# Kernel tuning notes

Hardware: AMD Instinct MI355X
Metric: run time of the kernel (lower is better)

The kernel has to match this reference:

```python
import jax, jax.numpy as jnp
import numpy as np

DIM = 1024      # internal_dim
HEADS = 16
HD = DIM // HEADS
M = 256         # meaning_dim (protected prefix)
E = 4           # num_experts
K = 2           # top_k
HID = 2048      # dim * ffn_mult
MID = 2048      # DeepNarrow mid = 2*dim
LB = 0.01
EPS = 1.1920929e-07  # torch.finfo(float32).eps (nn.RMSNorm default)


def _rms(x, w):
    return x * jax.lax.rsqrt(jnp.mean(x * x, axis=-1, keepdims=True) + EPS) * w


def _gelu(x):
    return jax.nn.gelu(x, approximate=False)  # F.gelu default (erf)


def setup_inputs() -> dict:
    key = jax.random.key(0)
    ks = jax.random.split(key, 20)
    d = DIM
    w = lambda k, s: (jax.random.normal(k, s, jnp.float32) * 0.02)
    return {
        "x": jax.random.normal(ks[0], (4, 1024, d), jnp.float32),
        "n1_w": jnp.ones((d,), jnp.float32),
        "n2_w": jnp.ones((d,), jnp.float32),
        "wq": w(ks[1], (d, d)), "wk": w(ks[2], (d, d)),
        "wv": w(ks[3], (d, d)), "wo": w(ks[4], (d, d)),
        "qn_w": jnp.ones((HD,), jnp.float32), "kn_w": jnp.ones((HD,), jnp.float32),
        "gate_w": w(ks[5], (E, d)),
        # expert 0: StandardFFN
        "e0_up": w(ks[6], (HID, d)), "e0_down": w(ks[7], (d, HID)),
        # expert 1: SwiGLUFFN
        "e1_w1": w(ks[8], (HID, d)), "e1_w2": w(ks[9], (HID, d)), "e1_down": w(ks[10], (d, HID)),
        # expert 2: DeepNarrowFFN
        "e2_l1": w(ks[11], (MID, d)), "e2_l2": w(ks[12], (HID, MID)),
        "e2_l3": w(ks[13], (MID, HID)), "e2_l4": w(ks[14], (d, MID)),
        # expert 3: BottleneckFFN (neck = dim)
        "e3_down": w(ks[15], (d, d)), "e3_up": w(ks[16], (HID, d)), "e3_out": w(ks[17], (d, HID)),
    }


def reference(x, n1_w, n2_w, wq, wk, wv, wo, qn_w, kn_w, gate_w,
              e0_up, e0_down, e1_w1, e1_w2, e1_down,
              e2_l1, e2_l2, e2_l3, e2_l4, e3_down, e3_up, e3_out):
    B, T, C = x.shape
    # ---- attention with QK-norm, causal (NoPE) ----
    h = _rms(x, n1_w)
    heads = lambda w_: (h @ w_.T).reshape(B, T, HEADS, HD).transpose(0, 2, 1, 3)  # [B,H,T,hd]
    q = _rms(heads(wq), qn_w)
    k = _rms(heads(wk), kn_w)
    v = heads(wv)
    scores = jnp.einsum('bhqd,bhkd->bhqk', q, k) * (HD ** -0.5)
    causal = jnp.tril(jnp.ones((T, T), bool))
    scores = jnp.where(causal[None, None], scores, -jnp.inf)
    attn = jax.nn.softmax(scores, axis=-1)
    ao = jnp.einsum('bhqk,bhkd->bhqd', attn, v).transpose(0, 2, 1, 3).reshape(B, T, C) @ wo.T
    ao = ao.at[:, :, :M].set(0.0)  # protect meaning dims
    x = x + ao
    # ---- heterogeneous MoE, top-k routing ----
    xf = _rms(x, n2_w).reshape(-1, C)  # [N,C]
    N = xf.shape[0]
    logits = jnp.nan_to_num(xf @ gate_w.T)
    probs = jax.nn.softmax(logits, axis=-1)
    topv, topi = jax.lax.top_k(probs, K)
    topv = topv / (topv.sum(-1, keepdims=True) + 1e-8)
    # dense per-token combine weights: zero for unselected experts (same math as dispatch loop)
    wts = jnp.zeros((N, E), x.dtype).at[jnp.arange(N)[:, None], topi].add(topv)
    o0 = _gelu(xf @ e0_up.T) @ e0_down.T
    o1 = (jax.nn.silu(xf @ e1_w1.T) * (xf @ e1_w2.T)) @ e1_down.T
    o2 = _gelu(_gelu(_gelu(xf @ e2_l1.T) @ e2_l2.T) @ e2_l3.T) @ e2_l4.T
    o3 = _gelu(_gelu(xf @ e3_down.T) @ e3_up.T) @ e3_out.T
    moe = (wts[:, 0:1] * o0 + wts[:, 1:2] * o1 + wts[:, 2:3] * o2 + wts[:, 3:4] * o3)
    moe = moe.reshape(B, T, C).at[:, :, :M].set(0.0)
    return x + moe
```

## Files before the change

kernel.cpp:

```cpp
#include <hip/hip_runtime.h>
#include <math.h>

#define DIM   1024
#define NTOK  4096
#define TSEQ  1024
#define NHEAD 16
#define MPROT 256
#define EPSR  1.1920929e-07f
#define SA    64.0f
#define SW    256.0f
#define SPC   64.0f

typedef __attribute__((ext_vector_type(8))) short          short8;
typedef __attribute__((ext_vector_type(8))) _Float16       half8;
typedef __attribute__((ext_vector_type(4))) _Float16       half4;
typedef __attribute__((ext_vector_type(4))) float          f32x4;
typedef __attribute__((ext_vector_type(4))) unsigned short us4;

static __device__ __forceinline__ float bf2f(unsigned short s) {
  union { unsigned int u; float f; } c; c.u = ((unsigned int)s) << 16; return c.f;
}
static __device__ __forceinline__ unsigned short f2bf(float f) {
  union { float f; unsigned int u; } c; c.f = f;
  return (unsigned short)((c.u + 0x7fffu + ((c.u >> 16) & 1u)) >> 16);
}
static __device__ __forceinline__ void gload16(void* lds, const void* g) {
  __builtin_amdgcn_global_load_lds(
      (__attribute__((address_space(1))) void*)const_cast<void*>(g),
      (__attribute__((address_space(3))) void*)lds, 16, 0, 0);
}

static __device__ __forceinline__ void tile_swz(int& m0, int& n0) {
  const int gx = gridDim.x;
  const int L = blockIdx.y * gx + blockIdx.x;
  const int xcd = L & 7;
  const int j = L >> 3;
  const int mbq = j / gx;
  const int nb = j - mbq * gx;
  m0 = ((mbq << 3) | xcd) << 7;
  n0 = nb << 7;
}

__global__ __launch_bounds__(256) void cvt_attn4_k(const float* __restrict__ wq,
                                                   const float* __restrict__ wk,
                                                   const float* __restrict__ wv,
                                                   const float* __restrict__ wo,
                                                   _Float16* __restrict__ dh,
                                                   _Float16* __restrict__ dl) {
  const int wi = blockIdx.y;
  const float* s = (wi == 0) ? wq : (wi == 1) ? wk : (wi == 2) ? wv : wo;
  const int i = blockIdx.x * 256 + threadIdx.x;
  const size_t off4 = ((size_t)wi << 20) >> 2;
  const float4 v = ((const float4*)s)[i];
  float a0 = v.x * SW, a1 = v.y * SW, a2 = v.z * SW, a3 = v.w * SW;
  half4 hv, lv;
  _Float16 h0 = (_Float16)a0; hv[0] = h0; lv[0] = (_Float16)(a0 - (float)h0);
  _Float16 h1 = (_Float16)a1; hv[1] = h1; lv[1] = (_Float16)(a1 - (float)h1);
  _Float16 h2 = (_Float16)a2; hv[2] = h2; lv[2] = (_Float16)(a2 - (float)h2);
  _Float16 h3 = (_Float16)a3; hv[3] = h3; lv[3] = (_Float16)(a3 - (float)h3);
  ((half4*)dh)[off4 + i] = hv; ((half4*)dl)[off4 + i] = lv;
}

__global__ __launch_bounds__(256) void cvt_moe_all_k(
    const float* s0, const float* s1, const float* s2, const float* s3,
    const float* s4, const float* s5, const float* s6, const float* s7,
    const float* s8, const float* s9, const float* s10, const float* s11,
    unsigned short* __restrict__ dst) {
  const int n4tab[12] = {524288, 524288, 524288, 524288, 524288, 524288,
                         1048576, 1048576, 524288, 262144, 524288, 524288};
  const size_t offtab[12] = {0, 2097152, 4194304, 6291456, 8388608, 10485760,
                             12582912, 16777216, 20971520, 23068672, 24117248, 26214400};
  const int wi = blockIdx.y;
  const int i = blockIdx.x * 256 + threadIdx.x;
  if (i >= n4tab[wi]) return;
  const float* s;
  switch (wi) {
    case 0: s = s0; break; case 1: s = s1; break; case 2: s = s2; break;
    case 3: s = s3; break; case 4: s = s4; break; case 5: s = s5; break;
    case 6: s = s6; break; case 7: s = s7; break; case 8: s = s8; break;
    case 9: s = s9; break; case 10: s = s10; break; default: s = s11; break;
  }
  const float4 v = ((const float4*)s)[i];
  us4 o; o[0] = f2bf(v.x); o[1] = f2bf(v.y); o[2] = f2bf(v.z); o[3] = f2bf(v.w);
  ((us4*)(dst + offtab[wi]))[i] = o;
}

__global__ __launch_bounds__(256) void rms_split_k(const float* __restrict__ in,
                                                   const float* __restrict__ wgt,
                                                   _Float16* __restrict__ oh,
                                                   _Float16* __restrict__ ol) {
  const int row = blockIdx.x, tid = threadIdx.x;
  const float4 v = ((const float4*)(in + (size_t)row * DIM))[tid];
  float ss = v.x * v.x + v.y * v.y + v.z * v.z + v.w * v.w;
#pragma unroll
  for (int o = 32; o; o >>= 1) ss += __shfl_xor(ss, o);
  __shared__ float red[4];
  if ((tid & 63) == 0) red[tid >> 6] = ss;
  __syncthreads();
  const float sc = rsqrtf((red[0] + red[1] + red[2] + red[3]) * (1.0f / DIM) + EPSR) * SA;
  const float4 wv = ((const float4*)wgt)[tid];
  float a[4] = {v.x * sc * wv.x, v.y * sc * wv.y, v.z * sc * wv.z, v.w * sc * wv.w};
  half4 hv, lv;
#pragma unroll
  for (int j = 0; j < 4; ++j) {
    _Float16 hh = (_Float16)a[j]; hv[j] = hh; lv[j] = (_Float16)(a[j] - (float)hh);
  }
  ((half4*)(oh + (size_t)row * DIM))[tid] = hv;
  ((half4*)(ol + (size_t)row * DIM))[tid] = lv;
}

__global__ __launch_bounds__(256) void rmsgate_k(const float* __restrict__ x2,
                                                 const float* __restrict__ n2w,
                                                 const float* __restrict__ gw,
                                                 unsigned short* __restrict__ xfb,
                                                 float* __restrict__ wts,
                                                 float* __restrict__ moe) {
  const int row = blockIdx.x, tid = threadIdx.x;
  ((float4*)(moe + (size_t)row * DIM))[tid] = (float4){0.f, 0.f, 0.f, 0.f};
  const float4 v = ((const float4*)(x2 + (size_t)row * DIM))[tid];
  float ss = v.x * v.x + v.y * v.y + v.z * v.z + v.w * v.w;
#pragma unroll
  for (int o = 32; o; o >>= 1) ss += __shfl_xor(ss, o);
  __shared__ float red[4];
  __shared__ float redE[4][4];
  const int w = tid >> 6, lane = tid & 63;
  if (lane == 0) red[w] = ss;
  __syncthreads();
  const float sc = rsqrtf((red[0] + red[1] + red[2] + red[3]) * (1.0f / DIM) + EPSR);
  const float4 nw = ((const float4*)n2w)[tid];
  const float xn0 = v.x * sc * nw.x, xn1 = v.y * sc * nw.y;
  const float xn2 = v.z * sc * nw.z, xn3 = v.w * sc * nw.w;
  us4 ob; ob[0] = f2bf(xn0); ob[1] = f2bf(xn1); ob[2] = f2bf(xn2); ob[3] = f2bf(xn3);
  ((us4*)(xfb + (size_t)row * DIM))[tid] = ob;
#pragma unroll
  for (int e = 0; e < 4; ++e) {
    const float4 g = ((const float4*)(gw + (size_t)e * DIM))[tid];
    float d = xn0 * g.x + xn1 * g.y + xn2 * g.z + xn3 * g.w;
#pragma unroll
    for (int o = 32; o; o >>= 1) d += __shfl_xor(d, o);
    if (lane == 0) redE[w][e] = d;
  }
  __syncthreads();
  if (tid == 0) {
    float lg[4];
#pragma unroll
    for (int e = 0; e < 4; ++e) lg[e] = redE[0][e] + redE[1][e] + redE[2][e] + redE[3][e];
    const float mx = fmaxf(fmaxf(lg[0], lg[1]), fmaxf(lg[2], lg[3]));
    float pe[4]; float sum = 0.0f;
#pragma unroll
    for (int e = 0; e < 4; ++e) { pe[e] = __expf(lg[e] - mx); sum += pe[e]; }
#pragma unroll
    for (int e = 0; e < 4; ++e) pe[e] /= sum;
    int i1 = 0;
    for (int e = 1; e < 4; ++e) if (pe[e] > pe[i1]) i1 = e;
    int i2 = -1;
    for (int e = 0; e < 4; ++e) { if (e == i1) continue; if (i2 < 0 || pe[e] > pe[i2]) i2 = e; }
    const float s2 = pe[i1] + pe[i2] + 1e-8f;
    float o[4] = {0.f, 0.f, 0.f, 0.f};
    o[i1] = pe[i1] / s2; o[i2] = pe[i2] / s2;
    float4 r; r.x = o[0]; r.y = o[1]; r.z = o[2]; r.w = o[3];
    *(float4*)(wts + (size_t)row * 4) = r;
  }
}

__global__ __launch_bounds__(256) void qknorm2_k(_Float16* __restrict__ qh,
                                                 _Float16* __restrict__ ql,
                                                 _Float16* __restrict__ kh,
                                                 _Float16* __restrict__ kl,
                                                 const float* __restrict__ qnw,
                                                 const float* __restrict__ knw) {
  _Float16* ph; _Float16* pl; const float* wgt;
  if (blockIdx.y == 0) { ph = qh; pl = ql; wgt = qnw; }
  else { ph = kh; pl = kl; wgt = knw; }
  const int idx = (blockIdx.x << 2) + (threadIdx.x >> 6);
  const int lane = threadIdx.x & 63;
  const size_t off = ((size_t)idx << 6) + lane;
  const float v = (float)ph[off] + (float)pl[off];
  float ss = v * v;
#pragma unroll
  for (int o = 32; o; o >>= 1) ss += __shfl_xor(ss, o);
  const float sc = rsqrtf(ss * (1.0f / (64.0f * SA * SA)) + EPSR);
  const float nv = v * sc * wgt[lane];
  _Float16 hh = (_Float16)nv;
  ph[off] = hh; pl[off] = (_Float16)(nv - (float)hh);
}

__global__ __launch_bounds__(256) void route2_k(const float* __restrict__ wts,
                                                int* __restrict__ idxP,
                                                int* __restrict__ meta) {
  const int tid = threadIdx.x, w = tid >> 6, lane = tid & 63;
  __shared__ int wsum[4];
  __shared__ int baseS;
  int off = 0;
  for (int e = 0; e < 4; ++e) {
    if (tid == 0) baseS = 0;
    __syncthreads();
    for (int c = 0; c < 16; ++c) {
      const int tok = (c << 8) + tid;
      const bool pred = wts[(size_t)tok * 4 + e] > 0.0f;
      const unsigned long long m = __ballot(pred);
      const int lanepre = __popcll(m & ((1ull << lane) - 1ull));
      if (lane == 0) wsum[w] = __popcll(m);
      __syncthreads();
      int wpre = 0;
#pragma unroll
      for (int i = 0; i < 4; ++i) wpre += (i < w) ? wsum[i] : 0;
      const int tot = wsum[0] + wsum[1] + wsum[2] + wsum[3];
      if (pred) idxP[off + baseS + wpre + lanepre] = tok;
      __syncthreads();
      if (tid == 0) baseS += tot;
      __syncthreads();
    }
    const int cnt = baseS;
    const int padded = (cnt + 127) & ~127;
    for (int j = cnt + tid; j < padded; j += 256) idxP[off + j] = -1;
    if (tid == 0) meta[80 + e] = off;
    const int mb0 = off >> 7, nmb = padded >> 7;
    for (int j = tid; j < nmb; j += 256) meta[mb0 + j] = e;
    off += padded;
    __syncthreads();
  }
  for (int j = (off >> 7) + tid; j < 72; j += 256) meta[j] = -1;
}

struct SubOpP {
  const unsigned short* A;
  const unsigned short* Bw;
  unsigned short* outb;
  const unsigned short* other;
  int K, nbn, act, ep, gath;
};
struct PhaseP { SubOpP op[4]; };

__global__ __launch_bounds__(256, 4) void gemm_moe_k(PhaseP ph,
                                                     const int* __restrict__ meta,
                                                     const int* __restrict__ idxP,
                                                     const float* __restrict__ wts,
                                                     float* __restrict__ moe) {
  __shared__ unsigned short As[128][64];
  __shared__ unsigned short Bs[128][64];
  const int L = blockIdx.y * 16 + blockIdx.x;
  const int xcd = L & 7;
  const int j = L >> 3;
  const int nb = j & 15;
  const int mb = ((j >> 4) << 3) | xcd;
  const int e = meta[mb];
  if (e < 0) return;
  SubOpP op;
  switch (e) {
    case 0: op = ph.op[0]; break;
    case 1: op = ph.op[1]; break;
    case 2: op = ph.op[2]; break;
    default: op = ph.op[3]; break;
  }
  if (op.nbn == 0 || nb >= op.nbn) return;
  const int m0p = mb << 7;
  const int lr0 = m0p - meta[80 + e];
  const int n0 = nb << 7;
  const int F = op.nbn << 7;
  const int K = op.K;
  const int tid = threadIdx.x;
  const int w = tid >> 6, lane = tid & 63;
  const int wr = ((w >> 1) << 6), wc = ((w & 1) << 6);
  const int rr = lane & 15, kgl = lane >> 4;
  const int srow = tid >> 3, sslot = tid & 7;

  int grow[4];
#pragma unroll
  for (int i = 0; i < 4; ++i) {
    const int r = (i << 5) + srow;
    if (op.gath) {
      const int t = idxP[m0p + r];
      grow[i] = (t < 0) ? 0 : t;
    } else {
      grow[i] = lr0 + r;
    }
  }

  f32x4 acc[4][4];
#pragma unroll
  for (int a_ = 0; a_ < 4; ++a_)
#pragma unroll
    for (int b_ = 0; b_ < 4; ++b_) acc[a_][b_] = (f32x4){0.f, 0.f, 0.f, 0.f};

  const int KT = K >> 6;
  for (int kt = 0; kt < KT; ++kt) {
    const int k0 = kt << 6;
#pragma unroll
    for (int i = 0; i < 4; ++i) {
      const int r = (i << 5) + srow;
      const int ls = sslot ^ (r & 7);
      gload16(&As[(i << 5) + (w << 3)][0], op.A + (size_t)grow[i] * K + k0 + (ls << 3));
      gload16(&Bs[(i << 5) + (w << 3)][0], op.Bw + (size_t)(n0 + r) * K + k0 + (ls << 3));
    }
    __syncthreads();
    short8 af[4][2], bfr[4][2];
#pragma unroll
    for (int f = 0; f < 4; ++f) {
#pragma unroll
      for (int ks = 0; ks < 2; ++ks) {
        const int row = wr + (f << 4) + rr;
        const int kg = (ks << 2) + kgl;
        af[f][ks] = *(const short8*)&As[row][(kg ^ (row & 7)) << 3];
        const int col = wc + (f << 4) + rr;
        bfr[f][ks] = *(const short8*)&Bs[col][(kg ^ (col & 7)) << 3];
      }
    }
#pragma unroll
    for (int fi = 0; fi < 4; ++fi)
#pragma unroll
      for (int fj = 0; fj < 4; ++fj)
#pragma unroll
        for (int ks = 0; ks < 2; ++ks)
          acc[fi][fj] = __builtin_amdgcn_mfma_f32_16x16x32_bf16(
              af[fi][ks], bfr[fj][ks], acc[fi][fj], 0, 0, 0);
    __syncthreads();
  }
#pragma unroll
  for (int fi = 0; fi < 4; ++fi)
#pragma unroll
    for (int fj = 0; fj < 4; ++fj) {
      const int col = n0 + wc + (fj << 4) + rr;
#pragma unroll
      for (int r = 0; r < 4; ++r) {
        const int rl = wr + (fi << 4) + (kgl << 2) + r;
        float v = acc[fi][fj][r];
        if (op.act) v = 0.5f * v * (1.0f + erff(v * 0.70710678118654752f));
        if (op.ep == 0) {
          op.outb[(size_t)(lr0 + rl) * F + col] = f2bf(v);
        } else if (op.ep == 1) {
          const size_t off = (size_t)(lr0 + rl) * F + col;
          const float sv = v / (1.0f + __expf(-v));
          op.outb[off] = f2bf(sv * bf2f(op.other[off]));
        } else {
          const int tok = idxP[m0p + rl];
          if (tok >= 0)
            atomicAdd(&moe[(size_t)tok * DIM + col], wts[(size_t)tok * 4 + e] * v);
        }
      }
    }
}

template <int EP>
__global__ __launch_bounds__(256, 4) void gemm_split_k(
    const _Float16* __restrict__ Ah, const _Float16* __restrict__ Al,
    const _Float16* __restrict__ Bh, const _Float16* __restrict__ Bl,
    int K, int F,
    _Float16* __restrict__ Oh, _Float16* __restrict__ Ol, float oscale,
    const float* __restrict__ resid, float* __restrict__ outf,
    _Float16* __restrict__ K2h, _Float16* __restrict__ K2l,
    _Float16* __restrict__ V2h, _Float16* __restrict__ V2l) {
  __shared__ _Float16 AsH[128][32], AsL[128][32];
  __shared__ _Float16 BsH[128][32], BsL[128][32];
  const int tid = threadIdx.x;
  const int w = tid >> 6, lane = tid & 63;
  const int wr = ((w >> 1) << 6), wc = ((w & 1) << 6);
  int m0, n0;
  tile_swz(m0, n0);
  const int rr = lane & 15, kgl = lane >> 4;
  const int srow = tid >> 2, sslot = tid & 3;

  f32x4 acc[4][4];
#pragma unroll
  for (int a_ = 0; a_ < 4; ++a_)
#pragma unroll
    for (int b_ = 0; b_ < 4; ++b_) acc[a_][b_] = (f32x4){0.f, 0.f, 0.f, 0.f};

  const int KT = K >> 5;
  for (int kt = 0; kt < KT; ++kt) {
    const int k0 = kt << 5;
#pragma unroll
    for (int i = 0; i < 2; ++i) {
      const int r = (i << 6) + srow;
      const int ls = sslot ^ ((r >> 1) & 3);
      const size_t ga = (size_t)(m0 + r) * K + k0 + (ls << 3);
      const size_t gb = (size_t)(n0 + r) * K + k0 + (ls << 3);
      const int lr = (i << 6) + (w << 4);
      gload16(&AsH[lr][0], Ah + ga);
      gload16(&AsL[lr][0], Al + ga);
      gload16(&BsH[lr][0], Bh + gb);
      gload16(&BsL[lr][0], Bl + gb);
    }
    __syncthreads();
    half8 ah[4], al[4], bh[4], bl[4];
#pragma unroll
    for (int f = 0; f < 4; ++f) {
      const int row = wr + (f << 4) + rr;
      const int pa = (kgl ^ ((row >> 1) & 3)) << 3;
      ah[f] = *(const half8*)&AsH[row][pa];
      al[f] = *(const half8*)&AsL[row][pa];
      const int col = wc + (f << 4) + rr;
      const int pb = (kgl ^ ((col >> 1) & 3)) << 3;
      bh[f] = *(const half8*)&BsH[col][pb];
      bl[f] = *(const half8*)&BsL[col][pb];
    }
#pragma unroll
    for (int fi = 0; fi < 4; ++fi)
#pragma unroll
      for (int fj = 0; fj < 4; ++fj) {
        acc[fi][fj] = __builtin_amdgcn_mfma_f32_16x16x32_f16(ah[fi], bh[fj], acc[fi][fj], 0, 0, 0);
        acc[fi][fj] = __builtin_amdgcn_mfma_f32_16x16x32_f16(ah[fi], bl[fj], acc[fi][fj], 0, 0, 0);
        acc[fi][fj] = __builtin_amdgcn_mfma_f32_16x16x32_f16(al[fi], bh[fj], acc[fi][fj], 0, 0, 0);
      }
    __syncthreads();
  }
#pragma unroll
  for (int fi = 0; fi < 4; ++fi)
#pragma unroll
    for (int fj = 0; fj < 4; ++fj) {
      const int col = n0 + wc + (fj << 4) + rr;
      const int rowb = m0 + wr + (fi << 4) + (kgl << 2);
      if (EP == 3) {
        if (col < 2048) {
          _Float16* ph = (col < 1024) ? Oh : K2h;
          _Float16* pl = (col < 1024) ? Ol : K2l;
          const int c = col & 1023;
#pragma unroll
          for (int r = 0; r < 4; ++r) {
            const float v = acc[fi][fj][r] * oscale;
            const _Float16 hh2 = (_Float16)v;
            const size_t off = (size_t)(rowb + r) * DIM + c;
            ph[off] = hh2; pl[off] = (_Float16)(v - (float)hh2);
          }
        } else {
          const int c2 = col - 2048;
          half4 h4, l4;
#pragma unroll
          for (int r = 0; r < 4; ++r) {
            const float v = acc[fi][fj][r] * oscale;
            const _Float16 hh2 = (_Float16)v;
            h4[r] = hh2; l4[r] = (_Float16)(v - (float)hh2);
          }
          const size_t vt = ((size_t)((rowb >> 10) << 4) + (size_t)(c2 >> 6)) * 65536 +
                            (size_t)(c2 & 63) * 1024 + (size_t)(rowb & 1023);
          *(half4*)&V2h[vt] = h4;
          *(half4*)&V2l[vt] = l4;
        }
      } else {
#pragma unroll
        for (int r = 0; r < 4; ++r) {
          const size_t off = (size_t)(rowb + r) * F + col;
          const float v = acc[fi][fj][r] * oscale;
          outf[off] = resid[off] + (col >= MPROT ? v : 0.0f);
        }
      }
    }
}

__global__ __launch_bounds__(256, 2) void attn_k(
    const _Float16* __restrict__ Qh, const _Float16* __restrict__ Ql,
    const _Float16* __restrict__ Kh, const _Float16* __restrict__ Kl,
    const _Float16* __restrict__ Vth, const _Float16* __restrict__ Vtl,
    _Float16* __restrict__ Oh, _Float16* __restrict__ Ol) {
  __shared__ _Float16 Ksh[2][32][64], Ksl[2][32][64];
  __shared__ _Float16 Vsh[2][64][40], Vsl[2][64][40];
  __shared__ _Float16 Plh[4][16][40], Pll[4][16][40];
  const int n = blockIdx.x;
  const int qt = n >> 6;
  const int bh = ((n & 7) << 3) | ((n >> 3) & 7);
  const int b = bh >> 4, h = bh & 15;
  const int tid = threadIdx.x, w = tid >> 6, lane = tid & 63;
  const int rr = lane & 15, rg = lane >> 4;
  const size_t tokbase = (size_t)b * TSEQ;
  const int hcol = h << 6;
  const size_t vtbase = (size_t)bh << 16;
  const int q0w = (qt << 7) + (w << 5);
  const float sscale = 0.125f / (SA * SA);

  half8 qfh[2][2], qfl[2][2];
#pragma unroll
  for (int qf = 0; qf < 2; ++qf)
#pragma unroll
    for (int ks = 0; ks < 2; ++ks) {
      const size_t off = (tokbase + q0w + (qf << 4) + rr) * DIM + hcol + (ks << 5) + (rg << 3);
      qfh[qf][ks] = *(const half8*)&Qh[off];
      qfl[qf][ks] = *(const half8*)&Ql[off];
    }

  f32x4 oacc[2][4];
#pragma unroll
  for (int qf = 0; qf < 2; ++qf)
#pragma unroll
    for (int dg = 0; dg < 4; ++dg) oacc[qf][dg] = (f32x4){0.f, 0.f, 0.f, 0.f};
  float mreg[2] = {-INFINITY, -INFINITY}, lreg[2] = {0.f, 0.f};

  const int kr = (w << 3) + (lane >> 3);
  const int kswz = ((lane & 7) ^ (kr & 7)) << 3;
  const int vr = tid >> 2;
  const int vs = (tid & 3) << 3;

  const int ntiles = (qt + 1) << 2;

  {
    gload16(&Ksh[0][w << 3][0], &Kh[(tokbase + kr) * DIM + hcol + kswz]);
    gload16(&Ksl[0][w << 3][0], &Kl[(tokbase + kr) * DIM + hcol + kswz]);
    const half8 vvh = *(const half8*)&Vth[vtbase + (size_t)vr * TSEQ + vs];
    const half8 vvl = *(const half8*)&Vtl[vtbase + (size_t)vr * TSEQ + vs];
    *(half8*)&Vsh[0][vr][vs] = vvh;
    *(half8*)&Vsl[0][vr][vs] = vvl;
    __syncthreads();
  }

  for (int t = 0; t < ntiles; ++t) {
    const int cur = t & 1;
    const int kv0 = t << 5;
    const bool havenext = (t + 1 < ntiles);
    half8 nvh, nvl;
    if (havenext) {
      const int kn = kv0 + 32;
      gload16(&Ksh[cur ^ 1][w << 3][0], &Kh[(tokbase + kn + kr) * DIM + hcol + kswz]);
      gload16(&Ksl[cur ^ 1][w << 3][0], &Kl[(tokbase + kn + kr) * DIM + hcol + kswz]);
      nvh = *(const half8*)&Vth[vtbase + (size_t)vr * TSEQ + kn + vs];
      nvl = *(const half8*)&Vtl[vtbase + (size_t)vr * TSEQ + kn + vs];
    }
    if (kv0 <= q0w + 31) {
      half8 kfh[2][2], kfl[2][2];
#pragma unroll
      for (int kt = 0; kt < 2; ++kt)
#pragma unroll
        for (int ks = 0; ks < 2; ++ks) {
          const int row = (kt << 4) + rr;
          const int sw = ((((ks << 2) + rg)) ^ (row & 7)) << 3;
          kfh[kt][ks] = *(const half8*)&Ksh[cur][row][sw];
          kfl[kt][ks] = *(const half8*)&Ksl[cur][row][sw];
        }
#pragma unroll
      for (int qf = 0; qf < 2; ++qf) {
        if (kv0 > q0w + (qf << 4) + 15) continue;
        f32x4 st[2];
        st[0] = (f32x4){0.f, 0.f, 0.f, 0.f};
        st[1] = (f32x4){0.f, 0.f, 0.f, 0.f};
#pragma unroll
        for (int kt = 0; kt < 2; ++kt)
#pragma unroll
          for (int ks = 0; ks < 2; ++ks) {
            st[kt] = __builtin_amdgcn_mfma_f32_16x16x32_f16(kfh[kt][ks], qfh[qf][ks], st[kt], 0, 0, 0);
            st[kt] = __builtin_amdgcn_mfma_f32_16x16x32_f16(kfh[kt][ks], qfl[qf][ks], st[kt], 0, 0, 0);
            st[kt] = __builtin_amdgcn_mfma_f32_16x16x32_f16(kfl[kt][ks], qfh[qf][ks], st[kt], 0, 0, 0);
          }
        const int qg = q0w + (qf << 4) + rr;
        float s[2][4]; float mx = -INFINITY;
#pragma unroll
        for (int kt = 0; kt < 2; ++kt)
#pragma unroll
          for (int r = 0; r < 4; ++r) {
            float sv = st[kt][r] * sscale;
            if (kv0 + (kt << 4) + (rg << 2) + r > qg) sv = -INFINITY;
            s[kt][r] = sv; mx = fmaxf(mx, sv);
          }
        mx = fmaxf(mx, __shfl_xor(mx, 16));
        mx = fmaxf(mx, __shfl_xor(mx, 32));
        const float mn = fmaxf(mreg[qf], mx);
        const float al = __expf(mreg[qf] - mn);
        mreg[qf] = mn;
        float p[2][4]; float rs = 0.f;
#pragma unroll
        for (int kt = 0; kt < 2; ++kt)
#pragma unroll
          for (int r = 0; r < 4; ++r) { p[kt][r] = __expf(s[kt][r] - mn); rs += p[kt][r]; }
        rs += __shfl_xor(rs, 16);
        rs += __shfl_xor(rs, 32);
        lreg[qf] = lreg[qf] * al + rs;
#pragma unroll
        for (int kt = 0; kt < 2; ++kt) {
          half4 h4, l4;
#pragma unroll
          for (int r = 0; r < 4; ++r) {
            const float pv = p[kt][r] * SPC;
            const _Float16 ph = (_Float16)pv;
            h4[r] = ph; l4[r] = (_Float16)(pv - (float)ph);
          }
          *(half4*)&Plh[w][rr][(kt << 4) + (rg << 2)] = h4;
          *(half4*)&Pll[w][rr][(kt << 4) + (rg << 2)] = l4;
        }
        float alr[4];
#pragma unroll
        for (int r = 0; r < 4; ++r) alr[r] = __shfl(al, (lane & 48) | ((rg << 2) + r));
#pragma unroll
        for (int dg = 0; dg < 4; ++dg)
#pragma unroll
          for (int r = 0; r < 4; ++r) oacc[qf][dg][r] *= alr[r];
        const half8 pah = *(const half8*)&Plh[w][rr][rg << 3];
        const half8 pal = *(const half8*)&Pll[w][rr][rg << 3];
#pragma unroll
        for (int dg = 0; dg < 4; ++dg) {
          const half8 vfh2 = *(const half8*)&Vsh[cur][(dg << 4) + rr][rg << 3];
          const half8 vfl2 = *(const half8*)&Vsl[cur][(dg << 4) + rr][rg << 3];
          oacc[qf][dg] = __builtin_amdgcn_mfma_f32_16x16x32_f16(pah, vfh2, oacc[qf][dg], 0, 0, 0);
          oacc[qf][dg] = __builtin_amdgcn_mfma_f32_16x16x32_f16(pah, vfl2, oacc[qf][dg], 0, 0, 0);
          oacc[qf][dg] = __builtin_amdgcn_mfma_f32_16x16x32_f16(pal, vfh2, oacc[qf][dg], 0, 0, 0);
        }
      }
    }
    if (havenext) {
      *(half8*)&Vsh[cur ^ 1][vr][vs] = nvh;
      *(half8*)&Vsl[cur ^ 1][vr][vs] = nvl;
    }
    __syncthreads();
  }
#pragma unroll
  for (int qf = 0; qf < 2; ++qf) {
    float li[4];
#pragma unroll
    for (int r = 0; r < 4; ++r)
      li[r] = __shfl(lreg[qf], (lane & 48) | ((rg << 2) + r));
#pragma unroll
    for (int dg = 0; dg < 4; ++dg)
#pragma unroll
      for (int r = 0; r < 4; ++r) {
        const int qloc = (rg << 2) + r;
        const float ov = oacc[qf][dg][r] / (li[r] * SPC);
        const _Float16 hh2 = (_Float16)ov;
        const size_t off = (tokbase + q0w + (qf << 4) + qloc) * DIM + hcol + (dg << 4) + rr;
        Oh[off] = hh2;
        Ol[off] = (_Float16)(ov - (float)hh2);
      }
  }
}

__global__ __launch_bounds__(256) void comb_k(float* __restrict__ outp,
                                              const float* __restrict__ moe) {
  const size_t i = (size_t)blockIdx.x * 256 + threadIdx.x;
  const int c4 = (int)(i & 255);
  if (c4 >= 64) {
    float4 o = ((float4*)outp)[i];
    const float4 m = ((const float4*)moe)[i];
    o.x += m.x; o.y += m.y; o.z += m.z; o.w += m.w;
    ((float4*)outp)[i] = o;
  }
}

extern "C" void kernel_launch(void* const* d_in, const int* in_sizes, int n_in,
                              void* d_out, int out_size, void* d_ws, size_t ws_size,
                              hipStream_t stream) {
  (void)in_sizes; (void)n_in; (void)out_size; (void)ws_size;
  const float* x    = (const float*)d_in[0];
  const float* n1w  = (const float*)d_in[1];
  const float* n2w  = (const float*)d_in[2];
  const float* wq   = (const float*)d_in[3];
  const float* wk   = (const float*)d_in[4];
  const float* wv   = (const float*)d_in[5];
  const float* wo   = (const float*)d_in[6];
  const float* qnw  = (const float*)d_in[7];
  const float* knw  = (const float*)d_in[8];
  const float* gw   = (const float*)d_in[9];
  const float* moesrc[12] = {
    (const float*)d_in[10], (const float*)d_in[11],
    (const float*)d_in[12], (const float*)d_in[13], (const float*)d_in[14],
    (const float*)d_in[15], (const float*)d_in[16], (const float*)d_in[17], (const float*)d_in[18],
    (const float*)d_in[19], (const float*)d_in[20], (const float*)d_in[21]
  };
  float* outp = (float*)d_out;

  char* p = (char*)d_ws;
  auto alloc = [&](size_t bytes) { void* r = (void*)p; p += (bytes + 255) & ~(size_t)255; return r; };
  const size_t NC = (size_t)NTOK * DIM;
  _Float16* hh = (_Float16*)alloc(NC * 2);
  _Float16* hl = (_Float16*)alloc(NC * 2);
  _Float16* qh = (_Float16*)alloc(NC * 2);
  _Float16* ql = (_Float16*)alloc(NC * 2);
  _Float16* kh = (_Float16*)alloc(NC * 2);
  _Float16* kl = (_Float16*)alloc(NC * 2);
  _Float16* vth = (_Float16*)alloc(NC * 2);
  _Float16* vtl = (_Float16*)alloc(NC * 2);
  unsigned short* xfb = (unsigned short*)alloc(NC * 2);
  float* moe = (float*)alloc(NC * 4);
  float* wts = (float*)alloc((size_t)NTOK * 4 * 4);
  _Float16* awh = (_Float16*)alloc((size_t)4 * 1024 * 1024 * 2);
  _Float16* awl = (_Float16*)alloc((size_t)4 * 1024 * 1024 * 2);
  unsigned short* moeW = (unsigned short*)alloc((size_t)28311552 * 2);
  int* idxP = (int*)alloc((size_t)9216 * 4);
  int* meta = (int*)alloc(512);
  unsigned short* e0t = (unsigned short*)qh;
  unsigned short* e1a = (unsigned short*)kh;
  unsigned short* e2a = (unsigned short*)vth;
  unsigned short* e1b = (unsigned short*)alloc((size_t)NTOK * 2048 * 2);
  unsigned short* e2b = (unsigned short*)alloc((size_t)NTOK * 2048 * 2);
  unsigned short* e3a = (unsigned short*)alloc((size_t)NTOK * 1024 * 2);
  unsigned short* e3b = (unsigned short*)alloc((size_t)NTOK * 2048 * 2);
  unsigned short* e2c = e2a;

  const size_t moff[12] = {0, 2097152, 4194304, 6291456, 8388608, 10485760,
                           12582912, 16777216, 20971520, 23068672, 24117248, 26214400};
  auto mw = [&](int i) -> const unsigned short* { return moeW + moff[i]; };

  cvt_attn4_k<<<dim3(1024, 4), dim3(256), 0, stream>>>(wq, wk, wv, wo, awh, awl);
  cvt_moe_all_k<<<dim3(4096, 12), dim3(256), 0, stream>>>(
      moesrc[0], moesrc[1], moesrc[2], moesrc[3], moesrc[4], moesrc[5],
      moesrc[6], moesrc[7], moesrc[8], moesrc[9], moesrc[10], moesrc[11], moeW);
  const _Float16* woh = awh + (3 << 20); const _Float16* wol = awl + (3 << 20);

  rms_split_k<<<dim3(NTOK), dim3(256), 0, stream>>>(x, n1w, hh, hl);
  gemm_split_k<3><<<dim3(24, 32), dim3(256), 0, stream>>>(
      hh, hl, awh, awl, 1024, 3072, qh, ql, 1.0f / SW, nullptr, nullptr,
      kh, kl, vth, vtl);
  qknorm2_k<<<dim3(NTOK * NHEAD / 4, 2), dim3(256), 0, stream>>>(qh, ql, kh, kl, qnw, knw);
  attn_k<<<dim3(512), dim3(256), 0, stream>>>(qh, ql, kh, kl, vth, vtl, hh, hl);
  gemm_split_k<1><<<dim3(8, 32), dim3(256), 0, stream>>>(
      hh, hl, woh, wol, 1024, 1024, nullptr, nullptr, 1.0f / (SA * SW), x, outp,
      nullptr, nullptr, nullptr, nullptr);

  rmsgate_k<<<dim3(NTOK), dim3(256), 0, stream>>>(outp, n2w, gw, xfb, wts, moe);
  route2_k<<<dim3(1), dim3(256), 0, stream>>>(wts, idxP, meta);

  auto mk = [&](const unsigned short* A, const unsigned short* B, unsigned short* outb,
                const unsigned short* other, int K, int nbn, int act, int ep, int gath) {
    SubOpP s; s.A = A; s.Bw = B; s.outb = outb; s.other = other;
    s.K = K; s.nbn = nbn; s.act = act; s.ep = ep; s.gath = gath;
    return s;
  };
  const SubOpP none = mk(nullptr, nullptr, nullptr, nullptr, 1024, 0, 0, 0, 0);

  PhaseP p1;
  p1.op[0] = mk(xfb, mw(0), e0t, nullptr, 1024, 16, 1, 0, 1);
  p1.op[1] = mk(xfb, mw(3), e1a, nullptr, 1024, 16, 0, 0, 1);
  p1.op[2] = mk(xfb, mw(5), e2a, nullptr, 1024, 16, 1, 0, 1);
  p1.op[3] = none;
  gemm_moe_k<<<dim3(16, 72), dim3(256), 0, stream>>>(p1, meta, idxP, wts, moe);

  PhaseP p2;
  p2.op[0] = mk(e0t, mw(1), nullptr, nullptr, 2048, 8, 0, 2, 0);
  p2.op[1] = mk(xfb, mw(2), e1b, e1a, 1024, 16, 0, 1, 1);
  p2.op[2] = mk(e2a, mw(6), e2b, nullptr, 2048, 16, 1, 0, 0);
  p2.op[3] = mk(xfb, mw(9), e3a, nullptr, 1024, 8, 1, 0, 1);
  gemm_moe_k<<<dim3(16, 72), dim3(256), 0, stream>>>(p2, meta, idxP, wts, moe);

  PhaseP p3;
  p3.op[0] = none;
  p3.op[1] = mk(e1b, mw(4), nullptr, nullptr, 2048, 8, 0, 2, 0);
  p3.op[2] = mk(e2b, mw(7), e2c, nullptr, 2048, 16, 1, 0, 0);
  p3.op[3] = mk(e3a, mw(10), e3b, nullptr, 1024, 16, 1, 0, 0);
  gemm_moe_k<<<dim3(16, 72), dim3(256), 0, stream>>>(p3, meta, idxP, wts, moe);

  PhaseP p4;
  p4.op[0] = none;
  p4.op[1] = none;
  p4.op[2] = mk(e2c, mw(8), nullptr, nullptr, 2048, 8, 0, 2, 0);
  p4.op[3] = mk(e3b, mw(11), nullptr, nullptr, 2048, 8, 0, 2, 0);
  gemm_moe_k<<<dim3(16, 72), dim3(256), 0, stream>>>(p4, meta, idxP, wts, moe);

  comb_k<<<dim3(4096), dim3(256), 0, stream>>>(outp, moe);
}
```

Measured before the change: 638.4 us.

## Compact MoE GEMM work lists, split-K final projections, rebalance expert phases

The routing kernel now builds per-phase compact work lists of (m-block, n-block, k-part) items, bucketed per XCD, so MoE GEMM launches no longer spawn and early-exit many idle blocks. Down-projections with K=2048 that write into the moe accumulator are split into two K halves to add parallelism. Expert 3's chain is moved one phase earlier to balance work across the four phases. Split-K relies on the ep=2 epilogue accumulating atomically into moe, and the single-block router does more serial work.

```diff
diff --git a/kernel.cpp b/kernel.cpp
--- a/kernel.cpp
+++ b/kernel.cpp
@@ -10,6 +10,7 @@
 #define SA    64.0f
 #define SW    256.0f
 #define SPC   64.0f
+#define MAXI  160
 
 typedef __attribute__((ext_vector_type(8))) short          short8;
 typedef __attribute__((ext_vector_type(8))) _Float16       half8;
@@ -185,9 +186,13 @@
   ph[off] = hh; pl[off] = (_Float16)(nv - (float)hh);
 }
 
+struct MoeCfg { int nbn[4][4]; int ks[4][4]; };
+
 __global__ __launch_bounds__(256) void route2_k(const float* __restrict__ wts,
                                                 int* __restrict__ idxP,
-                                                int* __restrict__ meta) {
+                                                int* __restrict__ meta,
+                                                int* __restrict__ work,
+                                                MoeCfg cfg) {
   const int tid = threadIdx.x, w = tid >> 6, lane = tid & 63;
   __shared__ int wsum[4];
   __shared__ int baseS;
@@ -221,6 +226,24 @@
     __syncthreads();
   }
   for (int j = (off >> 7) + tid; j < 72; j += 256) meta[j] = -1;
+  for (int j = tid; j < 4 * 8 * MAXI; j += 256) work[j] = -1;
+  __syncthreads();
+  if (tid < 32) {
+    const int p = tid >> 3, x = tid & 7;
+    int* wb = work + p * (8 * MAXI);
+    int n = 0;
+    const int totmb = off >> 7;
+    for (int mb = x; mb < totmb; mb += 8) {
+      const int e = meta[mb];
+      const int nbn = cfg.nbn[p][e];
+      const int ks = cfg.ks[p][e];
+      for (int nb = 0; nb < nbn; ++nb)
+        for (int k = 0; k < ks; ++k) {
+          wb[n * 8 + x] = mb | (nb << 8) | (k << 16);
+          ++n;
+        }
+    }
+  }
 }
 
 struct SubOpP {
@@ -228,7 +251,7 @@
   const unsigned short* Bw;
   unsigned short* outb;
   const unsigned short* other;
-  int K, nbn, act, ep, gath;
+  int K, nbn, act, ep, gath, ks;
 };
 struct PhaseP { SubOpP op[4]; };
 
@@ -236,16 +259,16 @@
                                                      const int* __restrict__ meta,
                                                      const int* __restrict__ idxP,
                                                      const float* __restrict__ wts,
-                                                     float* __restrict__ moe) {
+                                                     float* __restrict__ moe,
+                                                     const int* __restrict__ wk) {
   __shared__ unsigned short As[128][64];
   __shared__ unsigned short Bs[128][64];
-  const int L = blockIdx.y * 16 + blockIdx.x;
-  const int xcd = L & 7;
-  const int j = L >> 3;
-  const int nb = j & 15;
-  const int mb = ((j >> 4) << 3) | xcd;
+  const int item = wk[blockIdx.y * 8 + blockIdx.x];
+  if (item < 0) return;
+  const int mb = item & 255;
+  const int nb = (item >> 8) & 255;
+  const int kpart = (item >> 16) & 3;
   const int e = meta[mb];
-  if (e < 0) return;
   SubOpP op;
   switch (e) {
     case 0: op = ph.op[0]; break;
@@ -253,7 +276,6 @@
     case 2: op = ph.op[2]; break;
     default: op = ph.op[3]; break;
   }
-  if (op.nbn == 0 || nb >= op.nbn) return;
   const int m0p = mb << 7;
   const int lr0 = m0p - meta[80 + e];
   const int n0 = nb << 7;
@@ -283,8 +305,9 @@
 #pragma unroll
     for (int b_ = 0; b_ < 4; ++b_) acc[a_][b_] = (f32x4){0.f, 0.f, 0.f, 0.f};
 
-  const int KT = K >> 6;
-  for (int kt = 0; kt < KT; ++kt) {
+  int kt0 = 0, ktN = K >> 6;
+  if (op.ks == 2) { const int hgt = ktN >> 1; kt0 = kpart * hgt; ktN = kt0 + hgt; }
+  for (int kt = kt0; kt < ktN; ++kt) {
     const int k0 = kt << 6;
 #pragma unroll
     for (int i = 0; i < 4; ++i) {
@@ -671,6 +694,7 @@
   unsigned short* moeW = (unsigned short*)alloc((size_t)28311552 * 2);
   int* idxP = (int*)alloc((size_t)9216 * 4);
   int* meta = (int*)alloc(512);
+  int* work = (int*)alloc((size_t)4 * 8 * MAXI * 4);
   unsigned short* e0t = (unsigned short*)qh;
   unsigned short* e1a = (unsigned short*)kh;
   unsigned short* e2a = (unsigned short*)vth;
@@ -701,43 +725,56 @@
       nullptr, nullptr, nullptr, nullptr);
 
   rmsgate_k<<<dim3(NTOK), dim3(256), 0, stream>>>(outp, n2w, gw, xfb, wts, moe);
-  route2_k<<<dim3(1), dim3(256), 0, stream>>>(wts, idxP, meta);
+
+  MoeCfg cfg;
+  const int nbn_tab[4][4] = {{16, 16, 16, 8},
+                             {8, 16, 16, 16},
+                             {0, 8, 16, 8},
+                             {0, 0, 8, 0}};
+  const int ks_tab[4][4]  = {{1, 1, 1, 1},
+                             {2, 1, 1, 1},
+                             {1, 2, 1, 2},
+                             {1, 1, 2, 1}};
+  for (int pp = 0; pp < 4; ++pp)
+    for (int ee = 0; ee < 4; ++ee) { cfg.nbn[pp][ee] = nbn_tab[pp][ee]; cfg.ks[pp][ee] = ks_tab[pp][ee]; }
+
+  route2_k<<<dim3(1), dim3(256), 0, stream>>>(wts, idxP, meta, work, cfg);
 
   auto mk = [&](const unsigned short* A, const unsigned short* B, unsigned short* outb,
-                const unsigned short* other, int K, int nbn, int act, int ep, int gath) {
+                const unsigned short* other, int K, int nbn, int act, int ep, int gath, int ks) {
     SubOpP s; s.A = A; s.Bw = B; s.outb = outb; s.other = other;
-    s.K = K; s.nbn = nbn; s.act = act; s.ep = ep; s.gath = gath;
+    s.K = K; s.nbn = nbn; s.act = act; s.ep = ep; s.gath = gath; s.ks = ks;
     return s;
   };
-  const SubOpP none = mk(nullptr, nullptr, nullptr, nullptr, 1024, 0, 0, 0, 0);
+  const SubOpP none = mk(nullptr, nullptr, nullptr, nullptr, 1024, 0, 0, 0, 0, 1);
 
   PhaseP p1;
-  p1.op[0] = mk(xfb, mw(0), e0t, nullptr, 1024, 16, 1, 0, 1);
-  p1.op[1] = mk(xfb, mw(3), e1a, nullptr, 1024, 16, 0, 0, 1);
-  p1.op[2] = mk(xfb, mw(5), e2a, nullptr, 1024, 16, 1, 0, 1);
-  p1.op[3] = none;
-  gemm_moe_k<<<dim3(16, 72), dim3(256), 0, stream>>>(p1, meta, idxP, wts, moe);
+  p1.op[0] = mk(xfb, mw(0), e0t, nullptr, 1024, 16, 1, 0, 1, 1);
+  p1.op[1] = mk(xfb, mw(3), e1a, nullptr, 1024, 16, 0, 0, 1, 1);
+  p1.op[2] = mk(xfb, mw(5), e2a, nullptr, 1024, 16, 1, 0, 1, 1);
+  p1.op[3] = mk(xfb, mw(9), e3a, nullptr, 1024, 8, 1, 0, 1, 1);
+  gemm_moe_k<<<dim3(8, MAXI), dim3(256), 0, stream>>>(p1, meta, idxP, wts, moe, work);
 
   PhaseP p2;
-  p2.op[0] = mk(e0t, mw(1), nullptr, nullptr, 2048, 8, 0, 2, 0);
-  p2.op[1] = mk(xfb, mw(2), e1b, e1a, 1024, 16, 0, 1, 1);
-  p2.op[2] = mk(e2a, mw(6), e2b, nullptr, 2048, 16, 1, 0, 0);
-  p2.op[3] = mk(xfb, mw(9), e3a, nullptr, 1024, 8, 1, 0, 1);
-  gemm_moe_k<<<dim3(16, 72), dim3(256), 0, stream>>>(p2, meta, idxP, wts, moe);
+  p2.op[0] = mk(e0t, mw(1), nullptr, nullptr, 2048, 8, 0, 2, 0, 2);
+  p2.op[1] = mk(xfb, mw(2), e1b, e1a, 1024, 16, 0, 1, 1, 1);
+  p2.op[2] = mk(e2a, mw(6), e2b, nullptr, 2048, 16, 1, 0, 0, 1);
+  p2.op[3] = mk(e3a, mw(10), e3b, nullptr, 1024, 16, 1, 0, 0, 1);
+  gemm_moe_k<<<dim3(8, MAXI), dim3(256), 0, stream>>>(p2, meta, idxP, wts, moe, work + 8 * MAXI);
 
   PhaseP p3;
   p3.op[0] = none;
-  p3.op[1] = mk(e1b, mw(4), nullptr, nullptr, 2048, 8, 0, 2, 0);
-  p3.op[2] = mk(e2b, mw(7), e2c, nullptr, 2048, 16, 1, 0, 0);
-  p3.op[3] = mk(e3a, mw(10), e3b, nullptr, 1024, 16, 1, 0, 0);
-  gemm_moe_k<<<dim3(16, 72), dim3(256), 0, stream>>>(p3, meta, idxP, wts, moe);
+  p3.op[1] = mk(e1b, mw(4), nullptr, nullptr, 2048, 8, 0, 2, 0, 2);
+  p3.op[2] = mk(e2b, mw(7), e2c, nullptr, 2048, 16, 1, 0, 0, 1);
+  p3.op[3] = mk(e3b, mw(11), nullptr, nullptr, 2048, 8, 0, 2, 0, 2);
+  gemm_moe_k<<<dim3(8, MAXI), dim3(256), 0, stream>>>(p3, meta, idxP, wts, moe, work + 16 * MAXI);
 
   PhaseP p4;
   p4.op[0] = none;
   p4.op[1] = none;
-  p4.op[2] = mk(e2c, mw(8), nullptr, nullptr, 2048, 8, 0, 2, 0);
-  p4.op[3] = mk(e3b, mw(11), nullptr, nullptr, 2048, 8, 0, 2, 0);
-  gemm_moe_k<<<dim3(16, 72), dim3(256), 0, stream>>>(p4, meta, idxP, wts, moe);
+  p4.op[2] = mk(e2c, mw(8), nullptr, nullptr, 2048, 8, 0, 2, 0, 2);
+  p4.op[3] = none;
+  gemm_moe_k<<<dim3(8, MAXI), dim3(256), 0, stream>>>(p4, meta, idxP, wts, moe, work + 24 * MAXI);
 
   comb_k<<<dim3(4096), dim3(256), 0, stream>>>(outp, moe);
 }
```

Result: no change. 633.7 us (-0.7%).
